# Kernel optimization log

Hardware: AMD Instinct MI355X
Metric: run time of the kernel (lower is better)

The kernel has to match this reference:

```python
import jax, jax.numpy as jnp
import numpy as np
import math

B, H, S, DK = 2, 16, 2048, 64

def setup_inputs() -> dict:
    key = jax.random.key(0)
    kq, kk, kv, km = jax.random.split(key, 4)
    q = jax.random.normal(kq, (B, H, S, DK), dtype=jnp.float32)
    k = jax.random.normal(kk, (B, H, S, DK), dtype=jnp.float32)
    v = jax.random.normal(kv, (B, H, S, DK), dtype=jnp.float32)
    mask = jax.random.randint(km, (1, 1, S, S), 0, 2).astype(jnp.bool_)
    return {"q": q, "k": k, "v": v, "mask": mask}

def reference(q, k, v, mask):
    d_k = q.shape[-1]
    # scores: [B,H,Sq,Sk]
    scores = jnp.einsum('bhqd,bhkd->bhqk', q, k) / math.sqrt(d_k)
    scores = jnp.where(mask, jnp.float32(-1e9), scores)
    # NOTE: original uses nn.Softmax(dim=2) -> softmax over the QUERY axis
    attn = jax.nn.softmax(scores, axis=2)
    out = jnp.einsum('bhqk,bhkd->bhqd', attn, v)
    return out
```

## Files before the change

### kernel.cpp

```cpp
#include <hip/hip_runtime.h>
#include <math.h>

#define S_LEN 2048
#define NCH   32
#define N_BH  32

typedef short bf16x8 __attribute__((ext_vector_type(8)));
typedef _Float16 f16x8 __attribute__((ext_vector_type(8)));
typedef float f32x4  __attribute__((ext_vector_type(4)));
typedef unsigned short u16;
typedef unsigned short u16x8 __attribute__((ext_vector_type(8)));
typedef unsigned long long u64;

#define MFMA32(a,b,c) __builtin_amdgcn_mfma_f32_16x16x32_bf16((a),(b),(c),0,0,0)
#define MFMAH(a,b,c)  __builtin_amdgcn_mfma_f32_16x16x32_f16((a),(b),(c),0,0,0)
#define EXP2(x) __builtin_amdgcn_exp2f(x)

#define SC        0.18033688011112042f
#define MASKED_L2 (-14.0f)

__device__ __forceinline__ u16 f2h(float x) {
  union { _Float16 h; u16 u; } v;
  v.h = (_Float16)x;
  return v.u;
}
__device__ __forceinline__ u16 f2bf_rne(float x) {
  unsigned u = __float_as_uint(x);
  return (u16)((u + 0x7FFF + ((u >> 16) & 1)) >> 16);
}
__device__ __forceinline__ void bfsplit(float x, u16& h, u16& l) {
  unsigned u = __float_as_uint(x);
  h = (u16)(u >> 16);
  float hf = __uint_as_float(u & 0xFFFF0000u);
  l = f2bf_rne(x - hf);
}

__global__ __launch_bounds__(256) void pack_mask(
    const int* __restrict__ mask, u64* __restrict__ bits) {
  const int word = blockIdx.x * 4 + (threadIdx.x >> 6);
  const int lane = threadIdx.x & 63;
  const int row = word >> 5, wc = word & 31;
  int m = mask[(size_t)row * S_LEN + wc * 64 + lane];
  u64 b = __ballot(m != 0);
  if (lane == 0) bits[word] = b;
}

__global__ __launch_bounds__(256) void prep_qk(
    const float* __restrict__ Q, const float* __restrict__ K,
    u16* __restrict__ qf, u16* __restrict__ kf) {
  const int tid = threadIdx.x;
  const int slot = tid & 15, r0 = tid >> 4;
  const size_t rowbase = (size_t)blockIdx.x * 64;
#pragma unroll
  for (int p = 0; p < 4; ++p) {
    const size_t row = rowbase + p * 16 + r0;
    const size_t dst = row * 64 + ((slot * 4) ^ (((int)row & 7) << 3));
    float4 xq = *(const float4*)(Q + row * 64 + slot * 4);
    *(ushort4*)(qf + dst) = make_ushort4(
        f2h(xq.x * SC), f2h(xq.y * SC), f2h(xq.z * SC), f2h(xq.w * SC));
    float4 xk = *(const float4*)(K + row * 64 + slot * 4);
    *(ushort4*)(kf + dst) = make_ushort4(
        f2h(xk.x), f2h(xk.y), f2h(xk.z), f2h(xk.w));
  }
}

__global__ __launch_bounds__(256) void prep_w(
    const float* __restrict__ V, const float* __restrict__ part,
    u16* __restrict__ w_t) {
  __shared__ __align__(16) u16 ts[4096];
  const int tid = threadIdx.x;
  const int kc = blockIdx.x, bh = blockIdx.y;
  const int k = tid >> 2, dblk = (tid & 3) * 16;
  const size_t ko = (size_t)bh * S_LEN + kc * 64 + k;
  const float lsum = part[ko] + part[65536 + ko];
  const float ilk = 1.0f / lsum;
  const float* vb = V + ko * 64 + dblk;
#pragma unroll
  for (int u = 0; u < 4; ++u) {
    float4 x = *(const float4*)(vb + u * 4);
    float xs[4] = {x.x, x.y, x.z, x.w};
#pragma unroll
    for (int e = 0; e < 4; ++e) {
      const int d = dblk + u * 4 + e;
      ts[d * 64 + (k ^ ((d & 7) << 3))] = f2h(xs[e] * ilk);
    }
  }
  __syncthreads();
  u16* dst = w_t + ((size_t)bh * NCH + kc) * 4096;
#pragma unroll
  for (int j = 0; j < 2; ++j)
    *(u16x8*)(dst + j * 2048 + tid * 8) = *(const u16x8*)(ts + j * 2048 + tid * 8);
}

__global__ __launch_bounds__(512, 4) void passA(
    const u16* __restrict__ qf, const u16* __restrict__ kf,
    const u64* __restrict__ mbits, float* __restrict__ part) {
  __shared__ __align__(16) u16 qbuf[4096];

  const int tid = threadIdx.x;
  const int lane = tid & 63;
  const int w = tid >> 6;
  const int c = lane & 15;
  const int g = lane >> 4;
  const int bx = blockIdx.x;
  const int bh = blockIdx.y;
  const int qp = blockIdx.z;

  const size_t bh_off = (size_t)bh * S_LEN * 64;
  const int swc = (c & 7) << 3;

  f16x8 ka[2][2];
#pragma unroll
  for (int t = 0; t < 2; ++t) {
    const int row = bx * 256 + w * 32 + t * 16 + c;
#pragma unroll
    for (int h = 0; h < 2; ++h)
      ka[t][h] = *(const f16x8*)(kf + bh_off + (size_t)row * 64
                                 + ((h * 32 + g * 8) ^ swc));
  }

  u16x8 stg = *(const u16x8*)(qf + bh_off + (size_t)(qp * 1024) * 64 + tid * 8);

  float lp[2][4] = {{0.f, 0.f, 0.f, 0.f}, {0.f, 0.f, 0.f, 0.f}};
  const int word = bx * 4 + (w >> 1);
  const int sh0 = (w & 1) * 32;

  for (int qs = 0; qs < 16; ++qs) {
    __syncthreads();
    *(u16x8*)(qbuf + tid * 8) = stg;
    __syncthreads();
    if (qs + 1 < 16)
      stg = *(const u16x8*)(qf + bh_off
            + (size_t)(qp * 1024 + (qs + 1) * 64) * 64 + tid * 8);

#pragma unroll
    for (int sub = 0; sub < 4; ++sub) {
      f16x8 fh[2];
      const int rb = sub * 1024 + c * 64;
#pragma unroll
      for (int h = 0; h < 2; ++h)
        fh[h] = *(const f16x8*)(qbuf + rb + ((h * 32 + g * 8) ^ swc));
      const int qrow = qp * 1024 + qs * 64 + sub * 16 + c;
      const u64 mw = mbits[(size_t)qrow * NCH + word];
#pragma unroll
      for (int t = 0; t < 2; ++t) {
        f32x4 acc = {0.f, 0.f, 0.f, 0.f};
        acc = MFMAH(ka[t][0], fh[0], acc);
        acc = MFMAH(ka[t][1], fh[1], acc);
        const unsigned nib = (unsigned)(mw >> (sh0 + t * 16 + g * 4)) & 0xFu;
#pragma unroll
        for (int r = 0; r < 4; ++r) {
          const float s = ((nib >> r) & 1) ? MASKED_L2 : acc[r];
          lp[t][r] += EXP2(s);
        }
      }
    }
  }

#pragma unroll
  for (int off = 1; off < 16; off <<= 1)
#pragma unroll
    for (int t = 0; t < 2; ++t)
#pragma unroll
      for (int r = 0; r < 4; ++r) lp[t][r] += __shfl_xor(lp[t][r], off, 64);
  if (c == 0) {
#pragma unroll
    for (int t = 0; t < 2; ++t) {
      float4 o = {lp[t][0], lp[t][1], lp[t][2], lp[t][3]};
      *(float4*)(part + (size_t)qp * 65536 + (size_t)bh * S_LEN
                 + bx * 256 + w * 32 + t * 16 + g * 4) = o;
    }
  }
}

__global__ __launch_bounds__(256, 4) void passC(
    const u16* __restrict__ qf, const u16* __restrict__ kf,
    const u16* __restrict__ w_t, const u64* __restrict__ mbits,
    float* __restrict__ out) {
  __shared__ __align__(16) u16 sbuf[8192];
  __shared__ __align__(16) u16 p_s[4096];

  const int tid = threadIdx.x;
  const int lane = tid & 63;
  const int w = tid >> 6;
  const int c = lane & 15;
  const int g = lane >> 4;
  const int qc = blockIdx.x;
  const int bh = blockIdx.y;

  const size_t bh_off = (size_t)bh * S_LEN * 64;
  const u16* tb_k = kf + bh_off;
  const u16* tb_w = w_t + (size_t)bh * NCH * 4096;
  const int swc = (c & 7) << 3;

  const int qrow = qc * 64 + w * 16 + c;
  f16x8 qb_[2];
#pragma unroll
  for (int h = 0; h < 2; ++h)
    qb_[h] = *(const f16x8*)(qf + bh_off + (size_t)qrow * 64
                             + ((h * 32 + g * 8) ^ swc));

  f32x4 oacc[4];
#pragma unroll
  for (int dt = 0; dt < 4; ++dt) oacc[dt] = (f32x4){0.f, 0.f, 0.f, 0.f};

  const int pbase = w * 1024 + c * 64;
  const int so = tid * 8;

  u16x8 stg[4];
#pragma unroll
  for (int j = 0; j < 2; ++j) {
    stg[0 + j] = *(const u16x8*)(tb_k + j * 2048 + so);
    stg[2 + j] = *(const u16x8*)(tb_w + j * 2048 + so);
  }

  for (int kc = 0; kc < NCH; ++kc) {
    __syncthreads();
#pragma unroll
    for (int j = 0; j < 2; ++j) {
      *(u16x8*)(sbuf + j * 2048 + so) = stg[0 + j];
      *(u16x8*)(sbuf + 4096 + j * 2048 + so) = stg[2 + j];
    }
    __syncthreads();
    if (kc + 1 < NCH) {
      const size_t nb = (size_t)(kc + 1) * 4096;
#pragma unroll
      for (int j = 0; j < 2; ++j) {
        stg[0 + j] = *(const u16x8*)(tb_k + nb + j * 2048 + so);
        stg[2 + j] = *(const u16x8*)(tb_w + nb + j * 2048 + so);
      }
    }

    const u64 mw = mbits[(size_t)qrow * NCH + kc];

#pragma unroll
    for (int kt = 0; kt < 4; ++kt) {
      const int kbase = (16 * kt + c) * 64;
      f16x8 ak0 = *(const f16x8*)(sbuf + kbase + ((0 * 32 + g * 8) ^ swc));
      f16x8 ak1 = *(const f16x8*)(sbuf + kbase + ((1 * 32 + g * 8) ^ swc));
      f32x4 acc = {0.f, 0.f, 0.f, 0.f};
      acc = MFMAH(ak0, qb_[0], acc);
      acc = MFMAH(ak1, qb_[1], acc);
      const unsigned nib = (unsigned)(mw >> (kt * 16 + g * 4)) & 0xFu;
      u16 pb[4];
#pragma unroll
      for (int r = 0; r < 4; ++r) {
        const float s = ((nib >> r) & 1) ? MASKED_L2 : acc[r];
        pb[r] = f2h(EXP2(s));
      }
      *(ushort4*)(p_s + pbase + ((kt * 16 + g * 4) ^ swc)) =
          make_ushort4(pb[0], pb[1], pb[2], pb[3]);
    }

#pragma unroll
    for (int s2 = 0; s2 < 2; ++s2) {
      const int koff = (s2 * 32 + g * 8) ^ swc;
      f16x8 pb8 = *(const f16x8*)(p_s + pbase + koff);
#pragma unroll
      for (int dt = 0; dt < 4; ++dt) {
        f16x8 av = *(const f16x8*)(sbuf + 4096 + (16 * dt + c) * 64 + koff);
        oacc[dt] = MFMAH(av, pb8, oacc[dt]);
      }
    }
  }

  float* ob = out + (bh_off + (size_t)qrow * 64);
#pragma unroll
  for (int dt = 0; dt < 4; ++dt) {
    float4 o = {oacc[dt][0], oacc[dt][1], oacc[dt][2], oacc[dt][3]};
    *(float4*)(ob + dt * 16 + g * 4) = o;
  }
}

__global__ __launch_bounds__(256) void passA_colsum(
    const float* __restrict__ Q, const float* __restrict__ K,
    const u64* __restrict__ mbits, float* __restrict__ il_out) {
  const int tid = threadIdx.x;
  const int lane = tid & 63;
  const int w = tid >> 6;
  const int c = lane & 15;
  const int g = lane >> 4;
  const int kc = blockIdx.x;
  const int bh = blockIdx.y;

  const float* Qb = Q + (size_t)bh * S_LEN * 64;
  const float* Kb = K + (size_t)bh * S_LEN * 64;

  bf16x8 kah[2], kal[2];
  {
    const int krow = kc * 64 + w * 16 + c;
#pragma unroll
    for (int h = 0; h < 2; ++h) {
      const float* src = Kb + (size_t)krow * 64 + h * 32 + g * 8;
      float4 x = *(const float4*)(src);
      float4 y = *(const float4*)(src + 4);
      float xs[8] = {x.x, x.y, x.z, x.w, y.x, y.y, y.z, y.w};
#pragma unroll
      for (int e = 0; e < 8; ++e) {
        u16 hh, ll; bfsplit(xs[e], hh, ll);
        kah[h][e] = (short)hh; kal[h][e] = (short)ll;
      }
    }
  }

  float lp[4] = {0.f, 0.f, 0.f, 0.f};
  const int shift = w * 16 + g * 4;

  for (int qs = 0; qs < S_LEN / 16; ++qs) {
    const int qrow = qs * 16 + c;
    bf16x8 qbh_[2], qbl_[2];
#pragma unroll
    for (int h = 0; h < 2; ++h) {
      const float* src = Qb + (size_t)qrow * 64 + h * 32 + g * 8;
      float4 x = *(const float4*)(src);
      float4 y = *(const float4*)(src + 4);
      float xs[8] = {x.x, x.y, x.z, x.w, y.x, y.y, y.z, y.w};
#pragma unroll
      for (int e = 0; e < 8; ++e) {
        u16 hh, ll; bfsplit(xs[e] * SC, hh, ll);
        qbh_[h][e] = (short)hh; qbl_[h][e] = (short)ll;
      }
    }
    f32x4 acc = {0.f, 0.f, 0.f, 0.f};
#pragma unroll
    for (int h = 0; h < 2; ++h) {
      acc = MFMA32(kah[h], qbh_[h], acc);
      acc = MFMA32(kal[h], qbh_[h], acc);
      acc = MFMA32(kah[h], qbl_[h], acc);
    }
    u64 mw = mbits[(size_t)qrow * NCH + kc];
    unsigned nib = (unsigned)(mw >> shift) & 0xFu;
#pragma unroll
    for (int r = 0; r < 4; ++r) {
      float s = ((nib >> r) & 1) ? MASKED_L2 : acc[r];
      lp[r] += exp2f(s);
    }
  }
#pragma unroll
  for (int off = 1; off < 16; off <<= 1)
#pragma unroll
    for (int r = 0; r < 4; ++r) lp[r] += __shfl_xor(lp[r], off, 64);
  if (c == 0) {
    float4 o = {1.f / lp[0], 1.f / lp[1], 1.f / lp[2], 1.f / lp[3]};
    *(float4*)(il_out + (size_t)bh * S_LEN + kc * 64 + w * 16 + g * 4) = o;
  }
}

__global__ __launch_bounds__(256) void passC_out(
    const float* __restrict__ Q, const float* __restrict__ K,
    const float* __restrict__ V, const u64* __restrict__ mbits,
    const float* __restrict__ il_in, float* __restrict__ out) {
  __shared__ u16 kh_s[4096];
  __shared__ u16 kl_s[4096];
  __shared__ u16 vt_s[4096];
  __shared__ u16 p_s[4096];

  const int tid = threadIdx.x;
  const int lane = tid & 63;
  const int w = tid >> 6;
  const int c = lane & 15;
  const int g = lane >> 4;
  const int qc = blockIdx.x;
  const int bh = blockIdx.y;

  const float* Qb = Q + (size_t)bh * S_LEN * 64;
  const float* Kb = K + (size_t)bh * S_LEN * 64;
  const float* Vb = V + (size_t)bh * S_LEN * 64;

  bf16x8 qbh_[2], qbl_[2];
  {
    const int qrow = qc * 64 + w * 16 + c;
#pragma unroll
    for (int h = 0; h < 2; ++h) {
      const float* src = Qb + (size_t)qrow * 64 + h * 32 + g * 8;
      float4 x = *(const float4*)(src);
      float4 y = *(const float4*)(src + 4);
      float xs[8] = {x.x, x.y, x.z, x.w, y.x, y.y, y.z, y.w};
#pragma unroll
      for (int e = 0; e < 8; ++e) {
        u16 hh, ll; bfsplit(xs[e] * SC, hh, ll);
        qbh_[h][e] = (short)hh; qbl_[h][e] = (short)ll;
      }
    }
  }

  f32x4 oacc[4];
#pragma unroll
  for (int dt = 0; dt < 4; ++dt) oacc[dt] = (f32x4){0.f, 0.f, 0.f, 0.f};

  const int slot = tid & 15, r0 = tid >> 4;
  const int kv = tid & 63, dblk = tid >> 6;
  const int swc = (c & 7) << 3;
  const int pbase = w * 1024 + c * 64;

  for (int kc = 0; kc < NCH; ++kc) {
    __syncthreads();
#pragma unroll
    for (int p = 0; p < 4; ++p) {
      const int row = p * 16 + r0;
      float4 kx = *(const float4*)(Kb + (size_t)(kc * 64 + row) * 64 + slot * 4);
      float xs[4] = {kx.x, kx.y, kx.z, kx.w};
      u16 ha[4], la[4];
#pragma unroll
      for (int e = 0; e < 4; ++e) bfsplit(xs[e], ha[e], la[e]);
      const int idx = row * 64 + ((slot * 4) ^ ((row & 7) << 3));
      *(ushort4*)(kh_s + idx) = make_ushort4(ha[0], ha[1], ha[2], ha[3]);
      *(ushort4*)(kl_s + idx) = make_ushort4(la[0], la[1], la[2], la[3]);
    }
    {
      const float ilk = il_in[(size_t)bh * S_LEN + kc * 64 + kv];
#pragma unroll
      for (int u = 0; u < 4; ++u) {
        float4 vv = *(const float4*)(Vb + (size_t)(kc * 64 + kv) * 64 + dblk * 16 + u * 4);
        float xs[4] = {vv.x, vv.y, vv.z, vv.w};
#pragma unroll
        for (int e = 0; e < 4; ++e) {
          const int d = dblk * 16 + u * 4 + e;
          vt_s[d * 64 + (kv ^ ((d & 7) << 3))] = f2bf_rne(xs[e] * ilk);
        }
      }
    }
    __syncthreads();

    const u64 mw = mbits[(size_t)(qc * 64 + w * 16 + c) * NCH + kc];

#pragma unroll
    for (int kt = 0; kt < 4; ++kt) {
      const int kbase = (16 * kt + c) * 64;
      bf16x8 akh[2], akl[2];
#pragma unroll
      for (int h = 0; h < 2; ++h) {
        const int off = (h * 32 + g * 8) ^ swc;
        akh[h] = *(const bf16x8*)(kh_s + kbase + off);
        akl[h] = *(const bf16x8*)(kl_s + kbase + off);
      }
      f32x4 acc = {0.f, 0.f, 0.f, 0.f};
#pragma unroll
      for (int h = 0; h < 2; ++h) {
        acc = MFMA32(akh[h], qbh_[h], acc);
        acc = MFMA32(akl[h], qbh_[h], acc);
        acc = MFMA32(akh[h], qbl_[h], acc);
      }
      const unsigned nib = (unsigned)(mw >> (kt * 16 + g * 4)) & 0xFu;
      u16 pb[4];
#pragma unroll
      for (int r = 0; r < 4; ++r) {
        const float s = ((nib >> r) & 1) ? MASKED_L2 : acc[r];
        pb[r] = f2bf_rne(exp2f(s));
      }
      *(ushort4*)(p_s + pbase + ((kt * 16 + g * 4) ^ swc)) =
          make_ushort4(pb[0], pb[1], pb[2], pb[3]);
    }
    __syncthreads();

#pragma unroll
    for (int s = 0; s < 2; ++s) {
      const int koff = (s * 32 + 8 * g) ^ swc;
      bf16x8 pb8 = *(const bf16x8*)(p_s + pbase + koff);
#pragma unroll
      for (int dt = 0; dt < 4; ++dt) {
        bf16x8 av = *(const bf16x8*)(vt_s + (16 * dt + c) * 64 + koff);
        oacc[dt] = MFMA32(av, pb8, oacc[dt]);
      }
    }
  }

  float* ob = out + ((size_t)bh * S_LEN + qc * 64 + w * 16 + c) * 64;
#pragma unroll
  for (int dt = 0; dt < 4; ++dt) {
    float4 o = {oacc[dt][0], oacc[dt][1], oacc[dt][2], oacc[dt][3]};
    *(float4*)(ob + dt * 16 + g * 4) = o;
  }
}

extern "C" void kernel_launch(void* const* d_in, const int* in_sizes, int n_in,
                              void* d_out, int out_size, void* d_ws, size_t ws_size,
                              hipStream_t stream) {
  (void)in_sizes; (void)n_in; (void)out_size;
  const float* q = (const float*)d_in[0];
  const float* k = (const float*)d_in[1];
  const float* v = (const float*)d_in[2];
  const int* mask = (const int*)d_in[3];
  float* out = (float*)d_out;

  u64* mbits = (u64*)d_ws;
  float* part = (float*)((char*)d_ws + 524288);
  const size_t PL = (size_t)N_BH * S_LEN * 64;
  u16* qf = (u16*)((char*)d_ws + 524288 + 1048576);
  u16* kf = qf + PL;
  u16* w_t = kf + PL;
  const size_t need = 524288 + 1048576 + 3 * PL * sizeof(u16);

  pack_mask<<<dim3(S_LEN * NCH / 4), 256, 0, stream>>>(mask, mbits);

  if (ws_size >= need) {
    prep_qk<<<dim3(1024), 256, 0, stream>>>(q, k, qf, kf);
    passA<<<dim3(8, N_BH, 2), 512, 0, stream>>>(qf, kf, mbits, part);
    prep_w<<<dim3(NCH, N_BH), 256, 0, stream>>>(v, part, w_t);
    passC<<<dim3(NCH, N_BH), 256, 0, stream>>>(qf, kf, w_t, mbits, out);
  } else {
    float* il = part;
    dim3 grid(NCH, N_BH);
    passA_colsum<<<grid, 256, 0, stream>>>(q, k, mbits, il);
    passC_out<<<grid, 256, 0, stream>>>(q, k, v, mbits, il, out);
  }
}
```

Before: 127.5 us.

## Process two query row tiles per wave in passC and feed P directly from registers

passC now has each wave handle 32 query rows (two 16-row tiles) instead of 16, so every K and V tile loaded into LDS is reused for twice as many queries, and the grid is halved to S_LEN/128 blocks per head. The exponentiated scores are no longer written to and reread from a shared-memory P buffer. They are kept in registers and fed directly into 16x16x16 f16 MFMAs, whose accumulator layout matches the score layout. This removes the p_s LDS round trip and its traffic, at the cost of more registers per thread, fewer blocks, and twice as many smaller MFMA instructions. The fallback kernels also change the masked score constant from -14 to -30, which slightly changes the numerics of that path.

```diff
diff --git a/kernel.cpp b/kernel.cpp
--- a/kernel.cpp
+++ b/kernel.cpp
@@ -7,6 +7,7 @@
 
 typedef short bf16x8 __attribute__((ext_vector_type(8)));
 typedef _Float16 f16x8 __attribute__((ext_vector_type(8)));
+typedef _Float16 f16x4 __attribute__((ext_vector_type(4)));
 typedef float f32x4  __attribute__((ext_vector_type(4)));
 typedef unsigned short u16;
 typedef unsigned short u16x8 __attribute__((ext_vector_type(8)));
@@ -15,6 +16,17 @@
 #define MFMA32(a,b,c) __builtin_amdgcn_mfma_f32_16x16x32_bf16((a),(b),(c),0,0,0)
 #define MFMAH(a,b,c)  __builtin_amdgcn_mfma_f32_16x16x32_f16((a),(b),(c),0,0,0)
 #define EXP2(x) __builtin_amdgcn_exp2f(x)
+
+__device__ __forceinline__ f32x4 mfma16(f16x4 a, f16x4 b, f32x4 c) {
+#if __has_builtin(__builtin_amdgcn_mfma_f32_16x16x16f16)
+  return __builtin_amdgcn_mfma_f32_16x16x16f16(a, b, c, 0, 0, 0);
+#else
+  const _Float16 z = (_Float16)0.0f;
+  f16x8 a8 = {a[0], a[1], a[2], a[3], z, z, z, z};
+  f16x8 b8 = {b[0], b[1], b[2], b[3], z, z, z, z};
+  return MFMAH(a8, b8, c);
+#endif
+}
 
 #define SC        0.18033688011112042f
 #define MASKED_L2 (-14.0f)
@@ -178,7 +190,6 @@
     const u16* __restrict__ w_t, const u64* __restrict__ mbits,
     float* __restrict__ out) {
   __shared__ __align__(16) u16 sbuf[8192];
-  __shared__ __align__(16) u16 p_s[4096];
 
   const int tid = threadIdx.x;
   const int lane = tid & 63;
@@ -193,18 +204,23 @@
   const u16* tb_w = w_t + (size_t)bh * NCH * 4096;
   const int swc = (c & 7) << 3;
 
-  const int qrow = qc * 64 + w * 16 + c;
-  f16x8 qb_[2];
-#pragma unroll
-  for (int h = 0; h < 2; ++h)
-    qb_[h] = *(const f16x8*)(qf + bh_off + (size_t)qrow * 64
-                             + ((h * 32 + g * 8) ^ swc));
-
-  f32x4 oacc[4];
-#pragma unroll
-  for (int dt = 0; dt < 4; ++dt) oacc[dt] = (f32x4){0.f, 0.f, 0.f, 0.f};
-
-  const int pbase = w * 1024 + c * 64;
+  int qrow[2];
+  f16x8 qb[2][2];
+#pragma unroll
+  for (int u = 0; u < 2; ++u) {
+    qrow[u] = qc * 128 + w * 32 + u * 16 + c;
+#pragma unroll
+    for (int h = 0; h < 2; ++h)
+      qb[u][h] = *(const f16x8*)(qf + bh_off + (size_t)qrow[u] * 64
+                                 + ((h * 32 + g * 8) ^ swc));
+  }
+
+  f32x4 oacc[2][4];
+#pragma unroll
+  for (int u = 0; u < 2; ++u)
+#pragma unroll
+    for (int dt = 0; dt < 4; ++dt) oacc[u][dt] = (f32x4){0.f, 0.f, 0.f, 0.f};
+
   const int so = tid * 8;
 
   u16x8 stg[4];
@@ -231,44 +247,48 @@
       }
     }
 
-    const u64 mw = mbits[(size_t)qrow * NCH + kc];
+    const u64 mw0 = mbits[(size_t)qrow[0] * NCH + kc];
+    const u64 mw1 = mbits[(size_t)qrow[1] * NCH + kc];
 
 #pragma unroll
     for (int kt = 0; kt < 4; ++kt) {
       const int kbase = (16 * kt + c) * 64;
-      f16x8 ak0 = *(const f16x8*)(sbuf + kbase + ((0 * 32 + g * 8) ^ swc));
-      f16x8 ak1 = *(const f16x8*)(sbuf + kbase + ((1 * 32 + g * 8) ^ swc));
-      f32x4 acc = {0.f, 0.f, 0.f, 0.f};
-      acc = MFMAH(ak0, qb_[0], acc);
-      acc = MFMAH(ak1, qb_[1], acc);
-      const unsigned nib = (unsigned)(mw >> (kt * 16 + g * 4)) & 0xFu;
-      u16 pb[4];
-#pragma unroll
-      for (int r = 0; r < 4; ++r) {
-        const float s = ((nib >> r) & 1) ? MASKED_L2 : acc[r];
-        pb[r] = f2h(EXP2(s));
-      }
-      *(ushort4*)(p_s + pbase + ((kt * 16 + g * 4) ^ swc)) =
-          make_ushort4(pb[0], pb[1], pb[2], pb[3]);
-    }
-
-#pragma unroll
-    for (int s2 = 0; s2 < 2; ++s2) {
-      const int koff = (s2 * 32 + g * 8) ^ swc;
-      f16x8 pb8 = *(const f16x8*)(p_s + pbase + koff);
+      f16x8 ak0 = *(const f16x8*)(sbuf + kbase + ((g * 8) ^ swc));
+      f16x8 ak1 = *(const f16x8*)(sbuf + kbase + ((32 + g * 8) ^ swc));
+      f16x4 pf0, pf1;
+#pragma unroll
+      for (int u = 0; u < 2; ++u) {
+        f32x4 acc = {0.f, 0.f, 0.f, 0.f};
+        acc = MFMAH(ak0, qb[u][0], acc);
+        acc = MFMAH(ak1, qb[u][1], acc);
+        const u64 mwu = u ? mw1 : mw0;
+        const unsigned nib = (unsigned)(mwu >> (kt * 16 + g * 4)) & 0xFu;
+        f16x4 pf;
+#pragma unroll
+        for (int r = 0; r < 4; ++r) {
+          const float s = ((nib >> r) & 1) ? MASKED_L2 : acc[r];
+          pf[r] = (_Float16)EXP2(s);
+        }
+        if (u == 0) pf0 = pf; else pf1 = pf;
+      }
 #pragma unroll
       for (int dt = 0; dt < 4; ++dt) {
-        f16x8 av = *(const f16x8*)(sbuf + 4096 + (16 * dt + c) * 64 + koff);
-        oacc[dt] = MFMAH(av, pb8, oacc[dt]);
-      }
-    }
-  }
-
-  float* ob = out + (bh_off + (size_t)qrow * 64);
-#pragma unroll
-  for (int dt = 0; dt < 4; ++dt) {
-    float4 o = {oacc[dt][0], oacc[dt][1], oacc[dt][2], oacc[dt][3]};
-    *(float4*)(ob + dt * 16 + g * 4) = o;
+        const int aoff = 4096 + (16 * dt + c) * 64 + ((16 * kt + 4 * g) ^ swc);
+        f16x4 av = *(const f16x4*)(sbuf + aoff);
+        oacc[0][dt] = mfma16(av, pf0, oacc[0][dt]);
+        oacc[1][dt] = mfma16(av, pf1, oacc[1][dt]);
+      }
+    }
+  }
+
+#pragma unroll
+  for (int u = 0; u < 2; ++u) {
+    float* ob = out + (bh_off + (size_t)qrow[u] * 64);
+#pragma unroll
+    for (int dt = 0; dt < 4; ++dt) {
+      float4 o = {oacc[u][dt][0], oacc[u][dt][1], oacc[u][dt][2], oacc[u][dt][3]};
+      *(float4*)(ob + dt * 16 + g * 4) = o;
+    }
   }
 }
 
@@ -332,7 +352,7 @@
     unsigned nib = (unsigned)(mw >> shift) & 0xFu;
 #pragma unroll
     for (int r = 0; r < 4; ++r) {
-      float s = ((nib >> r) & 1) ? MASKED_L2 : acc[r];
+      float s = ((nib >> r) & 1) ? -30.0f : acc[r];
       lp[r] += exp2f(s);
     }
   }
@@ -445,7 +465,7 @@
       u16 pb[4];
 #pragma unroll
       for (int r = 0; r < 4; ++r) {
-        const float s = ((nib >> r) & 1) ? MASKED_L2 : acc[r];
+        const float s = ((nib >> r) & 1) ? -30.0f : acc[r];
         pb[r] = f2bf_rne(exp2f(s));
       }
       *(ushort4*)(p_s + pbase + ((kt * 16 + g * 4) ^ swc)) =
@@ -497,7 +517,7 @@
     prep_qk<<<dim3(1024), 256, 0, stream>>>(q, k, qf, kf);
     passA<<<dim3(8, N_BH, 2), 512, 0, stream>>>(qf, kf, mbits, part);
     prep_w<<<dim3(NCH, N_BH), 256, 0, stream>>>(v, part, w_t);
-    passC<<<dim3(NCH, N_BH), 256, 0, stream>>>(qf, kf, w_t, mbits, out);
+    passC<<<dim3(S_LEN / 128, N_BH), 256, 0, stream>>>(qf, kf, w_t, mbits, out);
   } else {
     float* il = part;
     dim3 grid(NCH, N_BH);
```

Measured after the change: 131.8 us. +3.4%, slower.

## Split passA query range four ways and double-buffer passC LDS tiles

Applied to the files above, without the earlier changes.

passA now splits the query axis into four partial column sums instead of two. This doubles the grid size and raises the occupancy hint, so the GPU has more blocks to keep its CUs busy. prep_w sums all four partials. passC switches to double-buffered shared K/W tiles with a single barrier per iteration instead of two, so staging the next chunk overlaps with compute. The fallback kernels also change their masked log-score constant, but that path only runs when the workspace is too small.

```diff
diff --git a/kernel.cpp b/kernel.cpp
--- a/kernel.cpp
+++ b/kernel.cpp
@@ -72,7 +72,8 @@
   const int kc = blockIdx.x, bh = blockIdx.y;
   const int k = tid >> 2, dblk = (tid & 3) * 16;
   const size_t ko = (size_t)bh * S_LEN + kc * 64 + k;
-  const float lsum = part[ko] + part[65536 + ko];
+  const float lsum = part[ko] + part[65536 + ko]
+                   + part[131072 + ko] + part[196608 + ko];
   const float ilk = 1.0f / lsum;
   const float* vb = V + ko * 64 + dblk;
 #pragma unroll
@@ -92,7 +93,7 @@
     *(u16x8*)(dst + j * 2048 + tid * 8) = *(const u16x8*)(ts + j * 2048 + tid * 8);
 }
 
-__global__ __launch_bounds__(512, 4) void passA(
+__global__ __launch_bounds__(512, 8) void passA(
     const u16* __restrict__ qf, const u16* __restrict__ kf,
     const u64* __restrict__ mbits, float* __restrict__ part) {
   __shared__ __align__(16) u16 qbuf[4096];
@@ -119,19 +120,19 @@
                                  + ((h * 32 + g * 8) ^ swc));
   }
 
-  u16x8 stg = *(const u16x8*)(qf + bh_off + (size_t)(qp * 1024) * 64 + tid * 8);
+  u16x8 stg = *(const u16x8*)(qf + bh_off + (size_t)(qp * 512) * 64 + tid * 8);
 
   float lp[2][4] = {{0.f, 0.f, 0.f, 0.f}, {0.f, 0.f, 0.f, 0.f}};
   const int word = bx * 4 + (w >> 1);
   const int sh0 = (w & 1) * 32;
 
-  for (int qs = 0; qs < 16; ++qs) {
+  for (int qs = 0; qs < 8; ++qs) {
     __syncthreads();
     *(u16x8*)(qbuf + tid * 8) = stg;
     __syncthreads();
-    if (qs + 1 < 16)
+    if (qs + 1 < 8)
       stg = *(const u16x8*)(qf + bh_off
-            + (size_t)(qp * 1024 + (qs + 1) * 64) * 64 + tid * 8);
+            + (size_t)(qp * 512 + (qs + 1) * 64) * 64 + tid * 8);
 
 #pragma unroll
     for (int sub = 0; sub < 4; ++sub) {
@@ -140,7 +141,7 @@
 #pragma unroll
       for (int h = 0; h < 2; ++h)
         fh[h] = *(const f16x8*)(qbuf + rb + ((h * 32 + g * 8) ^ swc));
-      const int qrow = qp * 1024 + qs * 64 + sub * 16 + c;
+      const int qrow = qp * 512 + qs * 64 + sub * 16 + c;
       const u64 mw = mbits[(size_t)qrow * NCH + word];
 #pragma unroll
       for (int t = 0; t < 2; ++t) {
@@ -177,7 +178,7 @@
     const u16* __restrict__ qf, const u16* __restrict__ kf,
     const u16* __restrict__ w_t, const u64* __restrict__ mbits,
     float* __restrict__ out) {
-  __shared__ __align__(16) u16 sbuf[8192];
+  __shared__ __align__(16) u16 sbuf[2][8192];
   __shared__ __align__(16) u16 p_s[4096];
 
   const int tid = threadIdx.x;
@@ -213,15 +214,15 @@
     stg[0 + j] = *(const u16x8*)(tb_k + j * 2048 + so);
     stg[2 + j] = *(const u16x8*)(tb_w + j * 2048 + so);
   }
-
+#pragma unroll
+  for (int j = 0; j < 2; ++j) {
+    *(u16x8*)(&sbuf[0][0] + j * 2048 + so) = stg[0 + j];
+    *(u16x8*)(&sbuf[0][0] + 4096 + j * 2048 + so) = stg[2 + j];
+  }
+  __syncthreads();
+
+  int cur = 0;
   for (int kc = 0; kc < NCH; ++kc) {
-    __syncthreads();
-#pragma unroll
-    for (int j = 0; j < 2; ++j) {
-      *(u16x8*)(sbuf + j * 2048 + so) = stg[0 + j];
-      *(u16x8*)(sbuf + 4096 + j * 2048 + so) = stg[2 + j];
-    }
-    __syncthreads();
     if (kc + 1 < NCH) {
       const size_t nb = (size_t)(kc + 1) * 4096;
 #pragma unroll
@@ -231,13 +232,14 @@
       }
     }
 
+    const u16* bufc = &sbuf[cur][0];
     const u64 mw = mbits[(size_t)qrow * NCH + kc];
 
 #pragma unroll
     for (int kt = 0; kt < 4; ++kt) {
       const int kbase = (16 * kt + c) * 64;
-      f16x8 ak0 = *(const f16x8*)(sbuf + kbase + ((0 * 32 + g * 8) ^ swc));
-      f16x8 ak1 = *(const f16x8*)(sbuf + kbase + ((1 * 32 + g * 8) ^ swc));
+      f16x8 ak0 = *(const f16x8*)(bufc + kbase + ((g * 8) ^ swc));
+      f16x8 ak1 = *(const f16x8*)(bufc + kbase + ((32 + g * 8) ^ swc));
       f32x4 acc = {0.f, 0.f, 0.f, 0.f};
       acc = MFMAH(ak0, qb_[0], acc);
       acc = MFMAH(ak1, qb_[1], acc);
@@ -258,10 +260,21 @@
       f16x8 pb8 = *(const f16x8*)(p_s + pbase + koff);
 #pragma unroll
       for (int dt = 0; dt < 4; ++dt) {
-        f16x8 av = *(const f16x8*)(sbuf + 4096 + (16 * dt + c) * 64 + koff);
+        f16x8 av = *(const f16x8*)(bufc + 4096 + (16 * dt + c) * 64 + koff);
         oacc[dt] = MFMAH(av, pb8, oacc[dt]);
       }
     }
+
+    if (kc + 1 < NCH) {
+      u16* bufn = &sbuf[cur ^ 1][0];
+#pragma unroll
+      for (int j = 0; j < 2; ++j) {
+        *(u16x8*)(bufn + j * 2048 + so) = stg[0 + j];
+        *(u16x8*)(bufn + 4096 + j * 2048 + so) = stg[2 + j];
+      }
+    }
+    __syncthreads();
+    cur ^= 1;
   }
 
   float* ob = out + (bh_off + (size_t)qrow * 64);
@@ -332,7 +345,7 @@
     unsigned nib = (unsigned)(mw >> shift) & 0xFu;
 #pragma unroll
     for (int r = 0; r < 4; ++r) {
-      float s = ((nib >> r) & 1) ? MASKED_L2 : acc[r];
+      float s = ((nib >> r) & 1) ? -30.0f : acc[r];
       lp[r] += exp2f(s);
     }
   }
@@ -445,7 +458,7 @@
       u16 pb[4];
 #pragma unroll
       for (int r = 0; r < 4; ++r) {
-        const float s = ((nib >> r) & 1) ? MASKED_L2 : acc[r];
+        const float s = ((nib >> r) & 1) ? -30.0f : acc[r];
         pb[r] = f2bf_rne(exp2f(s));
       }
       *(ushort4*)(p_s + pbase + ((kt * 16 + g * 4) ^ swc)) =
@@ -495,7 +508,7 @@
 
   if (ws_size >= need) {
     prep_qk<<<dim3(1024), 256, 0, stream>>>(q, k, qf, kf);
-    passA<<<dim3(8, N_BH, 2), 512, 0, stream>>>(qf, kf, mbits, part);
+    passA<<<dim3(8, N_BH, 4), 512, 0, stream>>>(qf, kf, mbits, part);
     prep_w<<<dim3(NCH, N_BH), 256, 0, stream>>>(v, part, w_t);
     passC<<<dim3(NCH, N_BH), 256, 0, stream>>>(qf, kf, w_t, mbits, out);
   } else {
```

Result: slower. 164.0 us (+28.7%).
